# Performance work log

Measured on AMD Instinct MI355X. Metric: run time of the kernel, lower is better.

Reference implementation:

```python
import jax, jax.numpy as jnp
import numpy as np

B, S, D, H = 2, 2048, 1024, 16
DEPTH = D // H


def setup_inputs() -> dict:
    key = jax.random.key(0)
    ks = jax.random.split(key, 9)
    sc = 1.0 / np.sqrt(D)
    return {
        "x": jax.random.normal(ks[0], (B, S, D), dtype=jnp.float32),
        "wq": jax.random.normal(ks[1], (D, D), dtype=jnp.float32) * sc,
        "bq": jnp.zeros((D,), dtype=jnp.float32),
        "wk": jax.random.normal(ks[2], (D, D), dtype=jnp.float32) * sc,
        "bk": jnp.zeros((D,), dtype=jnp.float32),
        "wv": jax.random.normal(ks[3], (D, D), dtype=jnp.float32) * sc,
        "bv": jnp.zeros((D,), dtype=jnp.float32),
        "wo": jax.random.normal(ks[4], (D, D), dtype=jnp.float32) * sc,
        "bo": jnp.zeros((D,), dtype=jnp.float32),
    }


def _split_heads(t):
    # [B,S,D] -> [B,H,S,depth]
    return t.reshape(B, S, H, DEPTH).transpose(0, 2, 1, 3)


def reference(x, wq, bq, wk, bk, wv, bv, wo, bo):
    q = _split_heads(x @ wq + bq)
    k = _split_heads(x @ wk + bk)
    v = _split_heads(x @ wv + bv)
    scale = 1.0 / jnp.sqrt(jnp.asarray(DEPTH, dtype=x.dtype))
    logits = jnp.einsum("bhqd,bhkd->bhqk", q, k) * scale
    attn = jax.nn.relu(logits)  # ReLU replaces softmax
    ctx = jnp.einsum("bhqk,bhkd->bhqd", attn, v)
    concat = ctx.transpose(0, 2, 1, 3).reshape(B, S, D)
    out = concat @ wo + bo
    return out, attn
```

## Files before the change

kernel.cpp:

```cpp
#include <hip/hip_runtime.h>
#include <hip/hip_bf16.h>

constexpr int Bn = 2, Sn = 2048, Dn = 1024, Hn = 16, DEP = 64;
constexpr int NTOKn = Bn * Sn;

typedef __bf16 bf16x8 __attribute__((ext_vector_type(8)));
typedef float f32x4 __attribute__((ext_vector_type(4)));

__device__ __forceinline__ unsigned short f2bf(float f) {
    union { __hip_bfloat16 h; unsigned short u; } cv;
    cv.h = __float2bfloat16(f);
    return cv.u;
}

__device__ __forceinline__ void gll16(const void* g, void* l) {
    __builtin_amdgcn_global_load_lds(
        (const __attribute__((address_space(1))) unsigned int*)g,
        (__attribute__((address_space(3))) unsigned int*)l, 16, 0, 0);
}

__global__ __launch_bounds__(256) void k_cvt_x(const float* __restrict__ x,
                                               unsigned short* __restrict__ xb,
                                               int n) {
    int idx = (blockIdx.x * 256 + threadIdx.x) * 4;
    if (idx < n) {
        float4 v = *reinterpret_cast<const float4*>(x + idx);
        ushort4 o;
        o.x = f2bf(v.x); o.y = f2bf(v.y); o.z = f2bf(v.z); o.w = f2bf(v.w);
        *reinterpret_cast<ushort4*>(xb + idx) = o;
    }
}

__global__ __launch_bounds__(256) void k_tconv_w(const float* __restrict__ w0,
                                                 const float* __restrict__ w1,
                                                 const float* __restrict__ w2,
                                                 const float* __restrict__ w3,
                                                 unsigned short* __restrict__ t0,
                                                 unsigned short* __restrict__ t1,
                                                 unsigned short* __restrict__ t2,
                                                 unsigned short* __restrict__ t3) {
    const float* w; unsigned short* tp;
    switch (blockIdx.z) {
        case 0: w = w0; tp = t0; break;
        case 1: w = w1; tp = t1; break;
        case 2: w = w2; tp = t2; break;
        default: w = w3; tp = t3; break;
    }
    __shared__ unsigned short tile[64][65];
    const int k0 = blockIdx.x * 64, n0 = blockIdx.y * 64;
    const int t = threadIdx.x;
    const int c = t & 63, rb = t >> 6;
#pragma unroll
    for (int i = 0; i < 16; ++i) {
        int r = rb + i * 4;
        tile[r][c] = f2bf(w[(size_t)(k0 + r) * Dn + n0 + c]);
    }
    __syncthreads();
#pragma unroll
    for (int i = 0; i < 16; ++i) {
        int n = rb + i * 4;
        tp[(size_t)(n0 + n) * Dn + k0 + c] = tile[c][n];
    }
}

__global__ __launch_bounds__(256) void k_tr_v(const unsigned short* __restrict__ V,
                                              unsigned short* __restrict__ VT) {
    __shared__ unsigned short tile[64][65];
    const int s0 = blockIdx.x * 64;
    const int bh = blockIdx.y;
    const int b = bh >> 4, h = bh & 15;
    const int t = threadIdx.x;
    const int c = t & 63, rb = t >> 6;
#pragma unroll
    for (int i = 0; i < 16; ++i) {
        int r = rb + i * 4;
        tile[r][c] = V[(size_t)(b * Sn + s0 + r) * Dn + h * DEP + c];
    }
    __syncthreads();
#pragma unroll
    for (int i = 0; i < 16; ++i) {
        int d = rb + i * 4;
        VT[(size_t)(bh * DEP + d) * Sn + s0 + c] = tile[c][d];
    }
}

__global__ __launch_bounds__(512, 2) void k_qkv8(const unsigned short* __restrict__ A,
                                                 const unsigned short* __restrict__ Bt,
                                                 const float* __restrict__ bq,
                                                 const float* __restrict__ bk,
                                                 const float* __restrict__ bv,
                                                 unsigned short* __restrict__ qkv) {
    extern __shared__ char smem[];
    constexpr int K = 1024, NT = K / 64;

    const int t = threadIdx.x;
    const int w = t >> 6, l = t & 63;
    const int wm = w >> 2, wn = w & 3;
    const int m0 = blockIdx.x * 256;
    const int n0 = blockIdx.y * 256;
    const int z = n0 >> 10;

    const float* bias = (z == 0) ? bq : (z == 1 ? bk : bv);
    float biasv[4];
#pragma unroll
    for (int nf = 0; nf < 4; ++nf)
        biasv[nf] = bias[(n0 + wn * 64 + nf * 16 + (l & 15)) & 1023];

    int aoff[2], boff[2], ldsoff[2];
#pragma unroll
    for (int i = 0; i < 2; ++i) {
        const int idx = i * 512 + t;
        const int row = idx >> 2;
        const int s = ((idx & 3) - row - (row >> 2)) & 3;
        aoff[i] = (m0 + row) * K + s * 8;
        boff[i] = (n0 + row) * K + s * 8;
        ldsoff[i] = idx * 16;
    }

    f32x4 acc[8][4] = {};

#pragma unroll
    for (int kh = 0; kh < 2; ++kh) {
        if (kh == 0) {
#pragma unroll
            for (int i = 0; i < 2; ++i) gll16(A + aoff[i] + 0 * 64 + 0 * 32, smem + 0 + 0 + ldsoff[i]);
#pragma unroll
            for (int i = 0; i < 2; ++i) gll16(Bt + boff[i] + 0 * 64 + 0 * 32, smem + 65536 + 0 + ldsoff[i]);
        } else {
#pragma unroll
            for (int i = 0; i < 2; ++i) gll16(A + aoff[i] + 0 * 64 + 1 * 32, smem + 0 + 16384 + ldsoff[i]);
#pragma unroll
            for (int i = 0; i < 2; ++i) gll16(Bt + boff[i] + 0 * 64 + 1 * 32, smem + 65536 + 16384 + ldsoff[i]);
        }
    }

    for (int kb = 0; kb < NT; ++kb) {
        const int c = kb & 1;
        const int kn = (kb + 1 < NT) ? kb + 1 : NT - 1;
        const int cn = c ^ 1;
        const int Abase = c * 32768;
        const int Bbase = 65536 + c * 32768;
        const int AbaseN = cn * 32768;
        const int BbaseN = 65536 + cn * 32768;

        bf16x8 bf[4], af[4];

#pragma unroll
        for (int ph = 0; ph < 4; ++ph) {
            const int kk = ph >> 1;
            const int mb = (ph & 1) * 4;

            if ((ph & 1) == 0) {
                asm volatile("s_waitcnt vmcnt(4)" ::: "memory");
            }
            __builtin_amdgcn_s_barrier();
            __builtin_amdgcn_sched_barrier(0);

            if ((ph & 1) == 0) {
#pragma unroll
                for (int nf = 0; nf < 4; ++nf) {
                    const int row = wn * 64 + nf * 16 + (l & 15);
                    const int byte = Bbase + kk * 16384 + row * 64 +
                                     ((((l >> 4) + row + (row >> 2)) & 3) * 16);
                    bf[nf] = *reinterpret_cast<const bf16x8*>(smem + byte);
                }
            }
#pragma unroll
            for (int mfl = 0; mfl < 4; ++mfl) {
                const int row = wm * 128 + (mb + mfl) * 16 + (l & 15);
                const int byte = Abase + kk * 16384 + row * 64 +
                                 ((((l >> 4) + row + (row >> 2)) & 3) * 16);
                af[mfl] = *reinterpret_cast<const bf16x8*>(smem + byte);
            }

            {
                const int khs = ph >> 1;
                if ((ph & 1) == 0) {
#pragma unroll
                    for (int i = 0; i < 2; ++i)
                        gll16(A + aoff[i] + kn * 64 + khs * 32,
                              smem + AbaseN + khs * 16384 + ldsoff[i]);
                } else {
#pragma unroll
                    for (int i = 0; i < 2; ++i)
                        gll16(Bt + boff[i] + kn * 64 + khs * 32,
                              smem + BbaseN + khs * 16384 + ldsoff[i]);
                }
            }

            asm volatile("s_waitcnt lgkmcnt(0)" ::: "memory");
            __builtin_amdgcn_sched_barrier(0);
            __builtin_amdgcn_s_setprio(1);
#pragma unroll
            for (int mfl = 0; mfl < 4; ++mfl)
#pragma unroll
                for (int nf = 0; nf < 4; ++nf)
                    acc[mb + mfl][nf] = __builtin_amdgcn_mfma_f32_16x16x32_bf16(
                        af[mfl], bf[nf], acc[mb + mfl][nf], 0, 0, 0);
            __builtin_amdgcn_s_setprio(0);
        }
    }

    asm volatile("s_waitcnt vmcnt(0)" ::: "memory");

    unsigned short* outz = qkv + (size_t)z * NTOKn * Dn;
#pragma unroll
    for (int mf = 0; mf < 8; ++mf) {
        const int row = m0 + wm * 128 + mf * 16 + (l >> 4) * 4;
#pragma unroll
        for (int nf = 0; nf < 4; ++nf) {
            const int col = (n0 + wn * 64 + nf * 16 + (l & 15)) & 1023;
#pragma unroll
            for (int i = 0; i < 4; ++i)
                outz[(size_t)(row + i) * Dn + col] = f2bf(acc[mf][nf][i] + biasv[nf]);
        }
    }
}

__global__ __launch_bounds__(256) void k_gemm_op(const unsigned short* __restrict__ A,
                                                 const unsigned short* __restrict__ Bt,
                                                 const float* __restrict__ bias,
                                                 float* __restrict__ C,
                                                 int M, int N, int K) {
    __shared__ unsigned short As[128][32];
    __shared__ unsigned short Bs[128][32];
    const int t = threadIdx.x;
    const int w = t >> 6, l = t & 63;
    const int m0 = blockIdx.x * 128, n0 = blockIdx.y * 128;
    const int wr = (w >> 1) * 64, wc = (w & 1) * 64;

    const int lrow = t >> 2;
    const int lcol = (t & 3) * 8;
    const unsigned short* gA = A + (size_t)(m0 + lrow) * K + lcol;
    const unsigned short* gB = Bt + (size_t)(n0 + lrow) * K + lcol;
    unsigned short* lA = &As[0][0] + t * 8;
    unsigned short* lB = &Bs[0][0] + t * 8;

    f32x4 acc[4][4] = {};

    for (int k0 = 0; k0 < K; k0 += 32) {
        __syncthreads();
        gll16(gA + k0, lA);
        gll16(gA + (size_t)64 * K + k0, lA + 2048);
        gll16(gB + k0, lB);
        gll16(gB + (size_t)64 * K + k0, lB + 2048);
        __syncthreads();

        bf16x8 af[4], bfv[4];
#pragma unroll
        for (int i = 0; i < 4; ++i)
            af[i] = *reinterpret_cast<const bf16x8*>(&As[wr + i * 16 + (l & 15)][(l >> 4) * 8]);
#pragma unroll
        for (int i = 0; i < 4; ++i)
            bfv[i] = *reinterpret_cast<const bf16x8*>(&Bs[wc + i * 16 + (l & 15)][(l >> 4) * 8]);
#pragma unroll
        for (int mi = 0; mi < 4; ++mi)
#pragma unroll
            for (int ni = 0; ni < 4; ++ni)
                acc[mi][ni] =
                    __builtin_amdgcn_mfma_f32_16x16x32_bf16(af[mi], bfv[ni], acc[mi][ni], 0, 0, 0);
    }

#pragma unroll
    for (int mi = 0; mi < 4; ++mi) {
        const int row = m0 + wr + mi * 16 + (l >> 4) * 4;
#pragma unroll
        for (int ni = 0; ni < 4; ++ni) {
            const int col = n0 + wc + ni * 16 + (l & 15);
            const float bv = bias[col];
#pragma unroll
            for (int i = 0; i < 4; ++i)
                C[(size_t)(row + i) * N + col] = acc[mi][ni][i] + bv;
        }
    }
}

__global__ __launch_bounds__(256, 2) void k_attn(const unsigned short* __restrict__ Qb,
                                                 const unsigned short* __restrict__ Kb,
                                                 const unsigned short* __restrict__ VTb,
                                                 float* __restrict__ attn,
                                                 unsigned short* __restrict__ ctx) {
    __shared__ unsigned short Ks[128 * 64];
    __shared__ unsigned short Vs[64 * 128];
    __shared__ unsigned short Ps[4][32][136];

    const int t = threadIdx.x;
    const int w = t >> 6, l = t & 63;
    const int q0 = blockIdx.x * 128;
    const int bh = blockIdx.y;
    const int b = bh >> 4, h = bh & 15;
    const float scale = 0.125f;

    bf16x8 qf[2][2];
#pragma unroll
    for (int mi = 0; mi < 2; ++mi)
#pragma unroll
        for (int kk = 0; kk < 2; ++kk)
            qf[mi][kk] = *reinterpret_cast<const bf16x8*>(
                Qb + (size_t)(b * Sn + q0 + w * 32 + mi * 16 + (l & 15)) * Dn + h * DEP +
                kk * 32 + (l >> 4) * 8);

    const int krow = t >> 3;
    const int kcolswz = ((t & 7) * 8) ^ ((krow & 7) << 3);
    const int vrow = t >> 4;
    const int vcolswz = ((t & 15) * 8) ^ ((vrow & 7) << 3);
    unsigned short* lK = Ks + t * 8;
    unsigned short* lV = Vs + t * 8;

    f32x4 ctxa[2][4] = {};
    f32x4 sa[2][8];

    float* const abase = attn + (size_t)bh * Sn * Sn + (size_t)(q0 + w * 32) * Sn;

    auto STAGE = [&](int kb) {
#pragma unroll
        for (int is = 0; is < 4; ++is) {
            gll16(Kb + (size_t)(b * Sn + kb * 128 + is * 32 + krow) * Dn + h * DEP + kcolswz,
                  lK + is * 2048);
            gll16(VTb + (size_t)(bh * DEP + is * 16 + vrow) * Sn + kb * 128 + vcolswz,
                  lV + is * 2048);
        }
    };

    auto QKT = [&]() {
#pragma unroll
        for (int mi = 0; mi < 2; ++mi)
#pragma unroll
            for (int nj = 0; nj < 8; ++nj)
                sa[mi][nj] = (f32x4){0.f, 0.f, 0.f, 0.f};
#pragma unroll
        for (int nj = 0; nj < 8; ++nj) {
            const int kr = nj * 16 + (l & 15);
#pragma unroll
            for (int kk = 0; kk < 2; ++kk) {
                const int kidx = (kr * 64 + kk * 32 + (l >> 4) * 8) ^ ((kr & 7) << 3);
                const bf16x8 bfr = *reinterpret_cast<const bf16x8*>(Ks + kidx);
                sa[0][nj] = __builtin_amdgcn_mfma_f32_16x16x32_bf16(qf[0][kk], bfr, sa[0][nj], 0, 0, 0);
                sa[1][nj] = __builtin_amdgcn_mfma_f32_16x16x32_bf16(qf[1][kk], bfr, sa[1][nj], 0, 0, 0);
            }
        }
#pragma unroll
        for (int mi = 0; mi < 2; ++mi) {
#pragma unroll
            for (int nj = 0; nj < 8; ++nj) {
                f32x4 v = sa[mi][nj];
#pragma unroll
                for (int i = 0; i < 4; ++i) {
                    float p = v[i] * scale;
                    v[i] = p > 0.f ? p : 0.f;
                }
                sa[mi][nj] = v;
                const int kc = nj * 16 + (l & 15);
#pragma unroll
                for (int i = 0; i < 4; ++i)
                    Ps[w][mi * 16 + (l >> 4) * 4 + i][kc] = f2bf(v[i]);
            }
        }
    };

    auto PV = [&]() {
        bf16x8 pf[2][4];
#pragma unroll
        for (int mi = 0; mi < 2; ++mi)
#pragma unroll
            for (int kk = 0; kk < 4; ++kk)
                pf[mi][kk] = *reinterpret_cast<const bf16x8*>(
                    &Ps[w][mi * 16 + (l & 15)][kk * 32 + (l >> 4) * 8]);
#pragma unroll
        for (int nd = 0; nd < 4; ++nd) {
            const int vr = nd * 16 + (l & 15);
#pragma unroll
            for (int kk = 0; kk < 4; ++kk) {
                const int vidx = (vr * 128 + kk * 32 + (l >> 4) * 8) ^ ((vr & 7) << 3);
                const bf16x8 vfr = *reinterpret_cast<const bf16x8*>(Vs + vidx);
                ctxa[0][nd] = __builtin_amdgcn_mfma_f32_16x16x32_bf16(pf[0][kk], vfr, ctxa[0][nd], 0, 0, 0);
                ctxa[1][nd] = __builtin_amdgcn_mfma_f32_16x16x32_bf16(pf[1][kk], vfr, ctxa[1][nd], 0, 0, 0);
            }
        }
    };

    auto STORE_SA = [&](int kb) {
        float* arow = abase + kb * 128;
#pragma unroll
        for (int mi = 0; mi < 2; ++mi)
#pragma unroll
            for (int nj = 0; nj < 8; ++nj) {
                const int kc = nj * 16 + (l & 15);
#pragma unroll
                for (int i = 0; i < 4; ++i)
                    arow[(size_t)(mi * 16 + (l >> 4) * 4 + i) * Sn + kc] = sa[mi][nj][i];
            }
    };

    STAGE(0);
    asm volatile("s_waitcnt vmcnt(0)" ::: "memory");
    __builtin_amdgcn_s_barrier();
    __builtin_amdgcn_sched_barrier(0);
    QKT();
    PV();

    for (int kb = 1; kb < Sn / 128; ++kb) {
        asm volatile("s_waitcnt lgkmcnt(0)" ::: "memory");
        __builtin_amdgcn_s_barrier();
        __builtin_amdgcn_sched_barrier(0);
        STAGE(kb);
        asm volatile("" ::: "memory");
        STORE_SA(kb - 1);
        asm volatile("s_waitcnt vmcnt(63)" ::: "memory");
        __builtin_amdgcn_s_barrier();
        __builtin_amdgcn_sched_barrier(0);
        QKT();
        PV();
    }
    STORE_SA(Sn / 128 - 1);

#pragma unroll
    for (int mi = 0; mi < 2; ++mi) {
#pragma unroll
        for (int nd = 0; nd < 4; ++nd) {
            const int dc = nd * 16 + (l & 15);
#pragma unroll
            for (int i = 0; i < 4; ++i) {
                const int qr = q0 + w * 32 + mi * 16 + (l >> 4) * 4 + i;
                ctx[(size_t)(b * Sn + qr) * Dn + h * DEP + dc] = f2bf(ctxa[mi][nd][i]);
            }
        }
    }
}

extern "C" void kernel_launch(void* const* d_in, const int* in_sizes, int n_in,
                              void* d_out, int out_size, void* d_ws, size_t ws_size,
                              hipStream_t stream) {
    (void)in_sizes; (void)n_in; (void)out_size; (void)ws_size;
    const float* x  = (const float*)d_in[0];
    const float* wq = (const float*)d_in[1];
    const float* bq = (const float*)d_in[2];
    const float* wk = (const float*)d_in[3];
    const float* bk = (const float*)d_in[4];
    const float* wv = (const float*)d_in[5];
    const float* bv = (const float*)d_in[6];
    const float* wo = (const float*)d_in[7];
    const float* bo = (const float*)d_in[8];

    float* out  = (float*)d_out;
    float* attn = out + (size_t)Bn * Sn * Dn;

    char* ws = (char*)d_ws;
    unsigned short* xb = (unsigned short*)ws;  ws += (size_t)NTOKn * Dn * 2;
    unsigned short* wT = (unsigned short*)ws;  ws += (size_t)4 * Dn * Dn * 2;
    unsigned short* qkv = (unsigned short*)ws; ws += (size_t)3 * NTOKn * Dn * 2;
    unsigned short* vT = (unsigned short*)ws;  ws += (size_t)NTOKn * Dn * 2;
    unsigned short* ctx = (unsigned short*)ws;

    const size_t DD = (size_t)Dn * Dn;

    static bool attr_set = false;
    if (!attr_set) {
        hipFuncSetAttribute(reinterpret_cast<const void*>(k_qkv8),
                            hipFuncAttributeMaxDynamicSharedMemorySize, 131072);
        attr_set = true;
    }

    k_cvt_x<<<dim3(NTOKn * Dn / 4 / 256), 256, 0, stream>>>(x, xb, NTOKn * Dn);
    k_tconv_w<<<dim3(16, 16, 4), 256, 0, stream>>>(wq, wk, wv, wo,
                                                   wT, wT + DD, wT + 2 * DD, wT + 3 * DD);
    k_qkv8<<<dim3(16, 12), 512, 131072, stream>>>(xb, wT, bq, bk, bv, qkv);
    k_tr_v<<<dim3(32, 32), 256, 0, stream>>>(qkv + (size_t)2 * NTOKn * Dn, vT);
    k_attn<<<dim3(16, 32), 256, 0, stream>>>(qkv, qkv + (size_t)NTOKn * Dn, vT, attn, ctx);
    k_gemm_op<<<dim3(32, 8), 256, 0, stream>>>(ctx, wT + 3 * DD, bo, out, NTOKn, Dn, Dn);
}
```

Measured before the change: 215.1 us.

## Fuse prep kernels, remap attention blocks per XCD, use nontemporal attn stores

Merges the x conversion and the weight transpose-convert into one launch, which removes a kernel launch and its gap. Remaps attention workgroups so that each XCD handles the query tiles of the same few heads, improving K/V L2 reuse. The attention-probability stores become nontemporal, so the large fp32 attn output bypasses the caches, and the loop order is changed so each lane writes along a row. The remap assumes round-robin dispatch of workgroups across 8 XCDs.

```diff
diff --git a/kernel.cpp b/kernel.cpp
--- a/kernel.cpp
+++ b/kernel.cpp
@@ -19,36 +19,36 @@
         (__attribute__((address_space(3))) unsigned int*)l, 16, 0, 0);
 }
 
-__global__ __launch_bounds__(256) void k_cvt_x(const float* __restrict__ x,
-                                               unsigned short* __restrict__ xb,
-                                               int n) {
-    int idx = (blockIdx.x * 256 + threadIdx.x) * 4;
-    if (idx < n) {
+__global__ __launch_bounds__(256) void k_prep(const float* __restrict__ x,
+                                              const float* __restrict__ w0,
+                                              const float* __restrict__ w1,
+                                              const float* __restrict__ w2,
+                                              const float* __restrict__ w3,
+                                              unsigned short* __restrict__ xb,
+                                              unsigned short* __restrict__ t0,
+                                              unsigned short* __restrict__ t1,
+                                              unsigned short* __restrict__ t2,
+                                              unsigned short* __restrict__ t3) {
+    const int bid = blockIdx.x;
+    const int t = threadIdx.x;
+    if (bid < 4096) {
+        const int idx = (bid * 256 + t) * 4;
         float4 v = *reinterpret_cast<const float4*>(x + idx);
         ushort4 o;
         o.x = f2bf(v.x); o.y = f2bf(v.y); o.z = f2bf(v.z); o.w = f2bf(v.w);
         *reinterpret_cast<ushort4*>(xb + idx) = o;
-    }
-}
-
-__global__ __launch_bounds__(256) void k_tconv_w(const float* __restrict__ w0,
-                                                 const float* __restrict__ w1,
-                                                 const float* __restrict__ w2,
-                                                 const float* __restrict__ w3,
-                                                 unsigned short* __restrict__ t0,
-                                                 unsigned short* __restrict__ t1,
-                                                 unsigned short* __restrict__ t2,
-                                                 unsigned short* __restrict__ t3) {
+        return;
+    }
+    const int b2 = bid - 4096;
     const float* w; unsigned short* tp;
-    switch (blockIdx.z) {
+    switch (b2 >> 8) {
         case 0: w = w0; tp = t0; break;
         case 1: w = w1; tp = t1; break;
         case 2: w = w2; tp = t2; break;
         default: w = w3; tp = t3; break;
     }
     __shared__ unsigned short tile[64][65];
-    const int k0 = blockIdx.x * 64, n0 = blockIdx.y * 64;
-    const int t = threadIdx.x;
+    const int k0 = ((b2 & 255) >> 4) * 64, n0 = (b2 & 15) * 64;
     const int c = t & 63, rb = t >> 6;
 #pragma unroll
     for (int i = 0; i < 16; ++i) {
@@ -123,14 +123,14 @@
     for (int kh = 0; kh < 2; ++kh) {
         if (kh == 0) {
 #pragma unroll
-            for (int i = 0; i < 2; ++i) gll16(A + aoff[i] + 0 * 64 + 0 * 32, smem + 0 + 0 + ldsoff[i]);
-#pragma unroll
-            for (int i = 0; i < 2; ++i) gll16(Bt + boff[i] + 0 * 64 + 0 * 32, smem + 65536 + 0 + ldsoff[i]);
+            for (int i = 0; i < 2; ++i) gll16(A + aoff[i], smem + ldsoff[i]);
+#pragma unroll
+            for (int i = 0; i < 2; ++i) gll16(Bt + boff[i], smem + 65536 + ldsoff[i]);
         } else {
 #pragma unroll
-            for (int i = 0; i < 2; ++i) gll16(A + aoff[i] + 0 * 64 + 1 * 32, smem + 0 + 16384 + ldsoff[i]);
-#pragma unroll
-            for (int i = 0; i < 2; ++i) gll16(Bt + boff[i] + 0 * 64 + 1 * 32, smem + 65536 + 16384 + ldsoff[i]);
+            for (int i = 0; i < 2; ++i) gll16(A + aoff[i] + 32, smem + 16384 + ldsoff[i]);
+#pragma unroll
+            for (int i = 0; i < 2; ++i) gll16(Bt + boff[i] + 32, smem + 65536 + 16384 + ldsoff[i]);
         }
     }
 
@@ -286,8 +286,11 @@
 
     const int t = threadIdx.x;
     const int w = t >> 6, l = t & 63;
-    const int q0 = blockIdx.x * 128;
-    const int bh = blockIdx.y;
+
+    const int lin = blockIdx.x + 16 * blockIdx.y;
+    const int xcd = lin & 7, idx = lin >> 3;
+    const int bh = xcd * 4 + (idx >> 4);
+    const int q0 = (idx & 15) * 128;
     const int b = bh >> 4, h = bh & 15;
     const float scale = 0.125f;
 
@@ -384,11 +387,11 @@
 #pragma unroll
         for (int mi = 0; mi < 2; ++mi)
 #pragma unroll
-            for (int nj = 0; nj < 8; ++nj) {
-                const int kc = nj * 16 + (l & 15);
-#pragma unroll
-                for (int i = 0; i < 4; ++i)
-                    arow[(size_t)(mi * 16 + (l >> 4) * 4 + i) * Sn + kc] = sa[mi][nj][i];
+            for (int i = 0; i < 4; ++i) {
+                float* r = arow + (size_t)(mi * 16 + (l >> 4) * 4 + i) * Sn + (l & 15);
+#pragma unroll
+                for (int nj = 0; nj < 8; ++nj)
+                    __builtin_nontemporal_store(sa[mi][nj][i], r + nj * 16);
             }
     };
 
@@ -461,9 +464,8 @@
         attr_set = true;
     }
 
-    k_cvt_x<<<dim3(NTOKn * Dn / 4 / 256), 256, 0, stream>>>(x, xb, NTOKn * Dn);
-    k_tconv_w<<<dim3(16, 16, 4), 256, 0, stream>>>(wq, wk, wv, wo,
-                                                   wT, wT + DD, wT + 2 * DD, wT + 3 * DD);
+    k_prep<<<dim3(5120), 256, 0, stream>>>(x, wq, wk, wv, wo, xb,
+                                           wT, wT + DD, wT + 2 * DD, wT + 3 * DD);
     k_qkv8<<<dim3(16, 12), 512, 131072, stream>>>(xb, wT, bq, bk, bv, qkv);
     k_tr_v<<<dim3(32, 32), 256, 0, stream>>>(qkv + (size_t)2 * NTOKn * Dn, vT);
     k_attn<<<dim3(16, 32), 256, 0, stream>>>(qkv, qkv + (size_t)NTOKn * Dn, vT, attn, ctx);
```

After: 233.0 us. 1.08x slower.
